# Kernel optimization log

Measured on AMD Instinct MI355X. Metric: run time of the kernel, lower is better.

## Reference

```python
import jax, jax.numpy as jnp
import numpy as np

C = 64
CQ = C // 8


def setup_inputs() -> dict:
    key = jax.random.key(0)
    ks = jax.random.split(key, 8)
    x = jax.random.normal(ks[0], (8, C, 64, 64), dtype=jnp.float32)
    s = 1.0 / np.sqrt(C)
    Wq = jax.random.normal(ks[1], (CQ, C), dtype=jnp.float32) * s
    bq = jax.random.normal(ks[2], (CQ,), dtype=jnp.float32) * s
    Wk = jax.random.normal(ks[3], (CQ, C), dtype=jnp.float32) * s
    bk = jax.random.normal(ks[4], (CQ,), dtype=jnp.float32) * s
    Wv = jax.random.normal(ks[5], (C, C), dtype=jnp.float32) * s
    bv = jax.random.normal(ks[6], (C,), dtype=jnp.float32) * s
    gamma = jnp.array([0.5], dtype=jnp.float32)  # nonzero so value path contributes
    return {"x": x, "Wq": Wq, "bq": bq, "Wk": Wk, "bk": bk, "Wv": Wv, "bv": bv, "gamma": gamma}


def reference(x, Wq, bq, Wk, bk, Wv, bv, gamma):
    B, Cc, H, W = x.shape
    xf = x.reshape(B, Cc, H * W)  # [B, C, N]
    # 1x1 conv == channel-mixing linear
    f = jnp.einsum('oc,bcn->bon', Wq, xf) + bq[None, :, None]  # [B, C/8, N]
    g = jnp.einsum('oc,bcn->bon', Wk, xf) + bk[None, :, None]  # [B, C/8, N]
    h = jnp.einsum('oc,bcn->bon', Wv, xf) + bv[None, :, None]  # [B, C, N]
    # scores[b,i,j] = f[b,:,i] . g[b,:,j]; softmax over dim=1 (query dim i)
    scores = jnp.einsum('bdi,bdj->bij', f, g)  # [B, N, N]
    beta = jax.nn.softmax(scores, axis=1)
    o = gamma[0] * jnp.einsum('bcn,bnm->bcm', h, beta) + xf
    return o.reshape(B, Cc, H, W)
```

## Files before the change

kernel.cpp:

```cpp
#include <hip/hip_runtime.h>
#include <hip/hip_fp16.h>


typedef _Float16 half8_t __attribute__((ext_vector_type(8)));
typedef _Float16 half4_t __attribute__((ext_vector_type(4)));
typedef _Float16 half2_t __attribute__((ext_vector_type(2)));
typedef __fp16  fp16x2  __attribute__((ext_vector_type(2)));
typedef float float4_t __attribute__((ext_vector_type(4)));

#define NTOK 4096
#define PRH 72
#define LOG2E 1.44269504088896340736f

#if __has_builtin(__builtin_amdgcn_exp2f)
__device__ __forceinline__ float fexp2(float x) { return __builtin_amdgcn_exp2f(x); }
#else
__device__ __forceinline__ float fexp2(float x) { return exp2f(x); }
#endif

__device__ __forceinline__ half2_t pkcvt(float a, float b) {
    fp16x2 v = __builtin_amdgcn_cvt_pkrtz(a, b);
    return __builtin_bit_cast(half2_t, v);
}

#define GLDS(G, L) __builtin_amdgcn_global_load_lds(                            \
    (const __attribute__((address_space(1))) unsigned int*)(G),                 \
    (__attribute__((address_space(3))) unsigned int*)(L), 16, 0, 0)

__global__ __launch_bounds__(320) void proj_kernel(
    const float* __restrict__ x,
    const float* __restrict__ Wq, const float* __restrict__ bq,
    const float* __restrict__ Wk, const float* __restrict__ bk,
    const float* __restrict__ Wv, const float* __restrict__ bv,
    __half* __restrict__ fTR, __half* __restrict__ gT16, __half* __restrict__ hM)
{
    __shared__ __align__(16) _Float16 xh[32 * PRH];
    const int t      = threadIdx.x;
    const int blk    = blockIdx.x;
    const int b      = blockIdx.y;
    const int n0     = blk * 32;
    const int kt64   = blk >> 1;
    const int t4base = (blk & 1) * 2;

    if (t < 256) {
#pragma unroll
        for (int i = 0; i < 2; i++) {
            const int idx = t + i * 256;
            const int c = idx >> 3, f4 = idx & 7;
            float4 v = *(const float4*)(x + (((size_t)(b * 64 + c)) << 12) + n0 + f4 * 4);
            const int cs = c ^ ((f4 & 3) << 4);
            xh[(f4 * 4 + 0) * PRH + cs] = (_Float16)v.x;
            xh[(f4 * 4 + 1) * PRH + cs] = (_Float16)v.y;
            xh[(f4 * 4 + 2) * PRH + cs] = (_Float16)v.z;
            xh[(f4 * 4 + 3) * PRH + cs] = (_Float16)v.w;
        }
    }

    const int w    = t >> 6;
    const int lane = t & 63;
    const int q    = lane >> 4;
    const int ml   = lane & 15;

    const float* wrow;
    if (w == 0) wrow = (ml < 8) ? (Wq + ml * 64) : (Wk + (ml - 8) * 64);
    else        wrow = Wv + ((w - 1) * 16 + ml) * 64;
    half4_t afr[4];
#pragma unroll
    for (int ks = 0; ks < 4; ks++) {
        float4 wv4 = *(const float4*)(wrow + ks * 16 + q * 4);
        afr[ks] = (half4_t){(_Float16)wv4.x, (_Float16)wv4.y,
                            (_Float16)wv4.z, (_Float16)wv4.w};
    }
    float4 bias4;
    if (w == 0) bias4 = (q < 2) ? *(const float4*)(bq + q * 4)
                                : *(const float4*)(bk + (q - 2) * 4);
    else        bias4 = *(const float4*)(bv + (w - 1) * 16 + q * 4);

    __syncthreads();

#pragma unroll
    for (int cg = 0; cg < 2; cg++) {
        const int tok  = cg * 16 + ml;
        const int swz  = (tok >> 2) & 3;
        float4_t acc = (float4_t){0.f, 0.f, 0.f, 0.f};
#pragma unroll
        for (int ks = 0; ks < 4; ks++) {
            half4_t bfr = *(const half4_t*)(&xh[tok * PRH + ((ks ^ swz) * 16 + q * 4)]);
            acc = __builtin_amdgcn_mfma_f32_16x16x16f16(afr[ks], bfr, acc, 0, 0, 0);
        }
        acc[0] += bias4.x; acc[1] += bias4.y; acc[2] += bias4.z; acc[3] += bias4.w;
        const int gtok = n0 + tok;
        const int t4   = t4base + cg;

        if (w == 0) {
            __half* rec = fTR + ((size_t)b << 16) + (size_t)(kt64 * 16 + ml) * 64;
            if (q < 2) {
                half4_t fv = {(_Float16)(acc[0] * LOG2E), (_Float16)(acc[1] * LOG2E),
                              (_Float16)(acc[2] * LOG2E), (_Float16)(acc[3] * LOG2E)};
                *(half4_t*)(rec + q * 16 + t4 * 4) = fv;
            } else {
                half4_t cv = (half4_t){};
                if (q == 2) cv[0] = (_Float16)1.0f;
                *(half4_t*)(rec + q * 16 + t4 * 4) = cv;
            }
            float gn2p = acc[0] * acc[0] + acc[1] * acc[1] +
                         acc[2] * acc[2] + acc[3] * acc[3];
            float gn2 = gn2p + __shfl_xor(gn2p, 16, 64);
            if (q >= 2) {
                half4_t gv = {(_Float16)acc[0], (_Float16)acc[1],
                              (_Float16)acc[2], (_Float16)acc[3]};
                __half* gp = gT16 + (size_t)((b << 12) + gtok) * 16;
                *(half4_t*)(gp + (q - 2) * 4) = gv;
                if (q == 2) {
                    const float M = (LOG2E * 4.6f) * __builtin_sqrtf(gn2) + 1.0f;
                    *(half4_t*)(gp + 8) = (half4_t){(_Float16)(-M), 0, 0, 0};
                } else {
                    *(half4_t*)(gp + 12) = (half4_t){};
                }
            }
        } else {
            const int ch  = (w - 1) * 16 + q * 4;
            const int pos = ((t4 >> 1) << 5) + ((ml >> 2) << 3) + ((t4 & 1) << 2) + (ml & 3);
            const size_t rowbase = ((size_t)(b * 64 + ch) << 12) + (size_t)kt64 * 64 + pos;
#pragma unroll
            for (int r = 0; r < 4; r++)
                hM[rowbase + ((size_t)r << 12)] = __float2half(acc[r]);
        }
    }
}

#define PAIR(SEA, SOA, SEB, SOB, GOFF)                                          \
    {                                                                           \
        const _Float16* hp = hb + (GOFF);                                       \
        half8_t ah0 = *(const half8_t*)(hp);                                    \
        half8_t ah1 = *(const half8_t*)(hp + 1024);                             \
        half8_t ah2 = *(const half8_t*)(hp + 2048);                             \
        half8_t ah3 = *(const half8_t*)(hp + 3072);                             \
        float eA0 = fexp2(SEA[0]), eA1 = fexp2(SEA[1]),                         \
              eA2 = fexp2(SEA[2]), eA3 = fexp2(SEA[3]);                         \
        float oA0 = fexp2(SOA[0]), oA1 = fexp2(SOA[1]),                         \
              oA2 = fexp2(SOA[2]), oA3 = fexp2(SOA[3]);                         \
        float eB0 = fexp2(SEB[0]), eB1 = fexp2(SEB[1]),                         \
              eB2 = fexp2(SEB[2]), eB3 = fexp2(SEB[3]);                         \
        float oB0 = fexp2(SOB[0]), oB1 = fexp2(SOB[1]),                         \
              oB2 = fexp2(SOB[2]), oB3 = fexp2(SOB[3]);                         \
        half2_t eaA = pkcvt(eA0, eA1), ebA = pkcvt(eA2, eA3);                   \
        half2_t oaA = pkcvt(oA0, oA1), obA = pkcvt(oA2, oA3);                   \
        half2_t eaB = pkcvt(eB0, eB1), ebB = pkcvt(eB2, eB3);                   \
        half2_t oaB = pkcvt(oB0, oB1), obB = pkcvt(oB2, oB3);                   \
        half8_t pA8 = {eaA[0], eaA[1], ebA[0], ebA[1],                          \
                       oaA[0], oaA[1], obA[0], obA[1]};                         \
        half8_t pB8 = {eaB[0], eaB[1], ebB[0], ebB[1],                          \
                       oaB[0], oaB[1], obB[0], obB[1]};                         \
        __builtin_amdgcn_s_setprio(1);                                          \
        accLA = __builtin_amdgcn_mfma_f32_16x16x32_f16(ones8, pA8, accLA, 0, 0, 0); \
        accLB = __builtin_amdgcn_mfma_f32_16x16x32_f16(ones8, pB8, accLB, 0, 0, 0); \
        accA[0] = __builtin_amdgcn_mfma_f32_16x16x32_f16(ah0, pA8, accA[0], 0, 0, 0); \
        accB[0] = __builtin_amdgcn_mfma_f32_16x16x32_f16(ah0, pB8, accB[0], 0, 0, 0); \
        accA[1] = __builtin_amdgcn_mfma_f32_16x16x32_f16(ah1, pA8, accA[1], 0, 0, 0); \
        accB[1] = __builtin_amdgcn_mfma_f32_16x16x32_f16(ah1, pB8, accB[1], 0, 0, 0); \
        accA[2] = __builtin_amdgcn_mfma_f32_16x16x32_f16(ah2, pA8, accA[2], 0, 0, 0); \
        accB[2] = __builtin_amdgcn_mfma_f32_16x16x32_f16(ah2, pB8, accB[2], 0, 0, 0); \
        accA[3] = __builtin_amdgcn_mfma_f32_16x16x32_f16(ah3, pA8, accA[3], 0, 0, 0); \
        accB[3] = __builtin_amdgcn_mfma_f32_16x16x32_f16(ah3, pB8, accB[3], 0, 0, 0); \
        __builtin_amdgcn_s_setprio(0);                                          \
    }

template<int NT>
__global__ __launch_bounds__(256) void attn_kernel(
    const __half* __restrict__ fTR, const __half* __restrict__ gT16,
    const __half* __restrict__ hM,
    __half* __restrict__ Pacc, float* __restrict__ Lsum)
{
    __shared__ __align__(16) _Float16 hl[2][4096];
    const int tid   = threadIdx.x;
    const int w     = tid >> 6;
    const int lane  = tid & 63;
    const int q     = lane >> 4;
    const int ml    = lane & 15;
    const int m7    = ml & 7;
    const int b     = blockIdx.y;
    const int split = blockIdx.z;
    const int colA  = blockIdx.x * 128 + w * 16 + ml;
    const int colB  = colA + 64;

    half4_t gfA = *(const half4_t*)(gT16 + ((size_t)((b << 12) + colA)) * 16 + q * 4);
    half4_t gfB = *(const half4_t*)(gT16 + ((size_t)((b << 12) + colB)) * 16 + q * 4);

    float4_t accA[4], accB[4];
#pragma unroll
    for (int cg = 0; cg < 4; cg++) {
        accA[cg] = (float4_t){0.f, 0.f, 0.f, 0.f};
        accB[cg] = (float4_t){0.f, 0.f, 0.f, 0.f};
    }
    float4_t accLA = (float4_t){0.f, 0.f, 0.f, 0.f};
    float4_t accLB = (float4_t){0.f, 0.f, 0.f, 0.f};
    const half8_t ones8 = {(_Float16)1.0f, (_Float16)1.0f, (_Float16)1.0f,
                           (_Float16)1.0f, (_Float16)1.0f, (_Float16)1.0f,
                           (_Float16)1.0f, (_Float16)1.0f};

    const int kt0 = split * NT;

    const int ch0  = tid >> 3;
    const int gsw  = (tid & 7) ^ (ch0 & 7);
    const __half* hs0 = hM + ((size_t)(b * 64 + ch0) << 12) + (size_t)kt0 * 64 + gsw * 8;
    const __half* hs1 = hs0 + ((size_t)32 << 12);
    const __half* fptr = fTR + ((size_t)b << 16) + (size_t)(kt0 * 16 + ml) * 64 + q * 16;

    const int gx0 = ((q ^ m7) << 3);
    const int gx1 = (((4 + q) ^ m7) << 3);

    GLDS(hs0, &hl[0][tid * 8]);
    GLDS(hs1, &hl[0][2048 + tid * 8]);
    half8_t f01 = *(const half8_t*)fptr;
    half8_t f23 = *(const half8_t*)(fptr + 8);
    __syncthreads();

#pragma unroll 1
    for (int kt = 0; kt < NT; kt++) {
        if (kt + 1 < NT) {
            _Float16* nb = &hl[(kt + 1) & 1][0];
            GLDS(hs0 + (kt + 1) * 64, nb + tid * 8);
            GLDS(hs1 + (kt + 1) * 64, nb + 2048 + tid * 8);
        }

        const _Float16* hb = &hl[kt & 1][ml << 6];
        half4_t afn0 = __builtin_shufflevector(f01, f01, 0, 1, 2, 3);
        half4_t afn1 = __builtin_shufflevector(f01, f01, 4, 5, 6, 7);
        half4_t afn2 = __builtin_shufflevector(f23, f23, 0, 1, 2, 3);
        half4_t afn3 = __builtin_shufflevector(f23, f23, 4, 5, 6, 7);

        __builtin_amdgcn_s_setprio(1);
        float4_t stA0 = __builtin_amdgcn_mfma_f32_16x16x16f16(
            afn0, gfA, (float4_t){0.f, 0.f, 0.f, 0.f}, 0, 0, 0);
        float4_t stA1 = __builtin_amdgcn_mfma_f32_16x16x16f16(
            afn1, gfA, (float4_t){0.f, 0.f, 0.f, 0.f}, 0, 0, 0);
        float4_t stA2 = __builtin_amdgcn_mfma_f32_16x16x16f16(
            afn2, gfA, (float4_t){0.f, 0.f, 0.f, 0.f}, 0, 0, 0);
        float4_t stA3 = __builtin_amdgcn_mfma_f32_16x16x16f16(
            afn3, gfA, (float4_t){0.f, 0.f, 0.f, 0.f}, 0, 0, 0);
        float4_t stB0 = __builtin_amdgcn_mfma_f32_16x16x16f16(
            afn0, gfB, (float4_t){0.f, 0.f, 0.f, 0.f}, 0, 0, 0);
        float4_t stB1 = __builtin_amdgcn_mfma_f32_16x16x16f16(
            afn1, gfB, (float4_t){0.f, 0.f, 0.f, 0.f}, 0, 0, 0);
        float4_t stB2 = __builtin_amdgcn_mfma_f32_16x16x16f16(
            afn2, gfB, (float4_t){0.f, 0.f, 0.f, 0.f}, 0, 0, 0);
        float4_t stB3 = __builtin_amdgcn_mfma_f32_16x16x16f16(
            afn3, gfB, (float4_t){0.f, 0.f, 0.f, 0.f}, 0, 0, 0);
        __builtin_amdgcn_s_setprio(0);

        if (kt + 1 < NT) {
            f01 = *(const half8_t*)(fptr + 1024);
            f23 = *(const half8_t*)(fptr + 1032);
            fptr += 1024;
        }

        PAIR(stA0, stA1, stB0, stB1, gx0)
        PAIR(stA2, stA3, stB2, stB3, gx1)

        __syncthreads();
    }

    __half* pa = Pacc + (((size_t)(split * 8 + b) * 64) << 12);
#pragma unroll
    for (int cg = 0; cg < 4; cg++)
#pragma unroll
        for (int r = 0; r < 4; r++) {
            int ch = cg * 16 + q * 4 + r;
            pa[((size_t)ch << 12) + colA] = __float2half(accA[cg][r]);
            pa[((size_t)ch << 12) + colB] = __float2half(accB[cg][r]);
        }
    if (q == 0) {
        Lsum[((size_t)(split * 8 + b) << 12) + colA] = accLA[0];
        Lsum[((size_t)(split * 8 + b) << 12) + colB] = accLB[0];
    }
}

template<int S>
__global__ __launch_bounds__(256) void merge_kernel(
    const __half* __restrict__ Pacc, const float* __restrict__ Lsum,
    const float* __restrict__ x, const float* __restrict__ gammap,
    float* __restrict__ out)
{
    __shared__ float invL[64];
    const int tid  = threadIdx.x;
    const int c4   = tid & 15;
    const int chh  = tid >> 4;
    const int b    = blockIdx.y;
    const int col0 = blockIdx.x * 64;
    const int ch   = blockIdx.z * 16 + chh;

    if (tid < 64) {
        float L = 0.f;
#pragma unroll
        for (int s = 0; s < S; s++)
            L += Lsum[((size_t)(s * 8 + b) << 12) + col0 + tid];
        invL[tid] = gammap[0] / L;
    }
    __syncthreads();

    const int cc = c4 * 4;
    const size_t base = (((size_t)b * 64 + ch) << 12) + col0 + cc;
    float4 xv = *(const float4*)(x + base);
    float o0 = 0.f, o1 = 0.f, o2 = 0.f, o3 = 0.f;
#pragma unroll
    for (int s = 0; s < S; s++) {
        half4_t pv = *(const half4_t*)(Pacc +
            (((size_t)(s * 8 + b) * 64 + ch) << 12) + col0 + cc);
        o0 += (float)pv[0];
        o1 += (float)pv[1];
        o2 += (float)pv[2];
        o3 += (float)pv[3];
    }
    float4 ov;
    ov.x = o0 * invL[cc]     + xv.x;
    ov.y = o1 * invL[cc + 1] + xv.y;
    ov.z = o2 * invL[cc + 2] + xv.z;
    ov.w = o3 * invL[cc + 3] + xv.w;
    *(float4*)(out + base) = ov;
}

extern "C" void kernel_launch(void* const* d_in, const int* in_sizes, int n_in,
                              void* d_out, int out_size, void* d_ws, size_t ws_size,
                              hipStream_t stream) {
    const float* x     = (const float*)d_in[0];
    const float* Wq    = (const float*)d_in[1];
    const float* bq    = (const float*)d_in[2];
    const float* Wk    = (const float*)d_in[3];
    const float* bk    = (const float*)d_in[4];
    const float* Wv    = (const float*)d_in[5];
    const float* bv    = (const float*)d_in[6];
    const float* gamma = (const float*)d_in[7];
    float* out = (float*)d_out;

    const size_t fr_bytes  = (size_t)8 * 65536 * 2;
    const size_t g_bytes   = (size_t)8 * NTOK * 16 * 2;
    const size_t hM_bytes  = (size_t)8 * 64 * NTOK * 2;
    const size_t pa_split  = (size_t)8 * 64 * NTOK * 2;
    const size_t l_split   = (size_t)8 * NTOK * sizeof(float);
    const size_t base_need = fr_bytes + g_bytes + hM_bytes;

    int S = 1;
    if (ws_size >= base_need + 8 * (pa_split + l_split)) S = 8;
    else if (ws_size >= base_need + 4 * (pa_split + l_split)) S = 4;
    else if (ws_size >= base_need + 2 * (pa_split + l_split)) S = 2;

    char* p = (char*)d_ws;
    __half* fTR  = (__half*)p;  p += fr_bytes;
    __half* gT16 = (__half*)p;  p += g_bytes;
    __half* hM   = (__half*)p;  p += hM_bytes;
    __half* Pacc = (__half*)p;  p += (size_t)S * pa_split;
    float*  Lsum = (float*)p;

    proj_kernel<<<dim3(128, 8), 320, 0, stream>>>(x, Wq, bq, Wk, bk, Wv, bv,
                                                  fTR, gT16, hM);
    if (S == 8) {
        attn_kernel<8><<<dim3(32, 8, 8), 256, 0, stream>>>(fTR, gT16, hM, Pacc, Lsum);
        merge_kernel<8><<<dim3(64, 8, 4), 256, 0, stream>>>(Pacc, Lsum, x, gamma, out);
    } else if (S == 4) {
        attn_kernel<16><<<dim3(32, 8, 4), 256, 0, stream>>>(fTR, gT16, hM, Pacc, Lsum);
        merge_kernel<4><<<dim3(64, 8, 4), 256, 0, stream>>>(Pacc, Lsum, x, gamma, out);
    } else if (S == 2) {
        attn_kernel<32><<<dim3(32, 8, 2), 256, 0, stream>>>(fTR, gT16, hM, Pacc, Lsum);
        merge_kernel<2><<<dim3(64, 8, 4), 256, 0, stream>>>(Pacc, Lsum, x, gamma, out);
    } else {
        attn_kernel<64><<<dim3(32, 8, 1), 256, 0, stream>>>(fTR, gT16, hM, Pacc, Lsum);
        merge_kernel<1><<<dim3(64, 8, 4), 256, 0, stream>>>(Pacc, Lsum, x, gamma, out);
    }
}
```

Baseline: 119.7 us.

## Triple-buffer attention LDS loads with vmcnt waits and drop 8-way split

Moves the attention kernel's value-tile staging from double to triple buffering in shared memory. Tiles are prefetched two iterations ahead, and the full __syncthreads is replaced by an explicit s_waitcnt vmcnt(2) plus s_barrier, so later loads can stay in flight while the current tile is consumed. It also removes the 8-way key split, so the maximum is 4 splits of 16 tiles each, which means fewer blocks and a smaller partial-sum merge. Shared memory per block grows and occupancy may drop; the vmcnt count relies on exactly how many loads are outstanding.

```diff
diff --git a/kernel.cpp b/kernel.cpp
--- a/kernel.cpp
+++ b/kernel.cpp
@@ -26,6 +26,13 @@
 #define GLDS(G, L) __builtin_amdgcn_global_load_lds(                            \
     (const __attribute__((address_space(1))) unsigned int*)(G),                 \
     (__attribute__((address_space(3))) unsigned int*)(L), 16, 0, 0)
+
+#define WAITVM2_BAR() do {                                                      \
+    __builtin_amdgcn_sched_barrier(0);                                          \
+    asm volatile("s_waitcnt vmcnt(2)" ::: "memory");                            \
+    __builtin_amdgcn_sched_barrier(0);                                          \
+    __builtin_amdgcn_s_barrier();                                               \
+} while (0)
 
 __global__ __launch_bounds__(320) void proj_kernel(
     const float* __restrict__ x,
@@ -172,7 +179,7 @@
     const __half* __restrict__ hM,
     __half* __restrict__ Pacc, float* __restrict__ Lsum)
 {
-    __shared__ __align__(16) _Float16 hl[2][4096];
+    __shared__ __align__(16) _Float16 hl[3][4096];
     const int tid   = threadIdx.x;
     const int w     = tid >> 6;
     const int lane  = tid & 63;
@@ -210,21 +217,21 @@
     const int gx0 = ((q ^ m7) << 3);
     const int gx1 = (((4 + q) ^ m7) << 3);
 
-    GLDS(hs0, &hl[0][tid * 8]);
-    GLDS(hs1, &hl[0][2048 + tid * 8]);
+    _Float16* bcur = &hl[0][0];
+    _Float16* bnxt = &hl[1][0];
+    _Float16* bnx2 = &hl[2][0];
+
+    GLDS(hs0, bcur + tid * 8);
+    GLDS(hs1, bcur + 2048 + tid * 8);
     half8_t f01 = *(const half8_t*)fptr;
     half8_t f23 = *(const half8_t*)(fptr + 8);
-    __syncthreads();
+    GLDS(hs0 + 64, bnxt + tid * 8);
+    GLDS(hs1 + 64, bnxt + 2048 + tid * 8);
+    WAITVM2_BAR();
 
 #pragma unroll 1
     for (int kt = 0; kt < NT; kt++) {
-        if (kt + 1 < NT) {
-            _Float16* nb = &hl[(kt + 1) & 1][0];
-            GLDS(hs0 + (kt + 1) * 64, nb + tid * 8);
-            GLDS(hs1 + (kt + 1) * 64, nb + 2048 + tid * 8);
-        }
-
-        const _Float16* hb = &hl[kt & 1][ml << 6];
+        const _Float16* hb = bcur + (ml << 6);
         half4_t afn0 = __builtin_shufflevector(f01, f01, 0, 1, 2, 3);
         half4_t afn1 = __builtin_shufflevector(f01, f01, 4, 5, 6, 7);
         half4_t afn2 = __builtin_shufflevector(f23, f23, 0, 1, 2, 3);
@@ -254,11 +261,18 @@
             f23 = *(const half8_t*)(fptr + 1032);
             fptr += 1024;
         }
+        if (kt + 2 < NT) {
+            GLDS(hs0 + (kt + 2) * 64, bnx2 + tid * 8);
+            GLDS(hs1 + (kt + 2) * 64, bnx2 + 2048 + tid * 8);
+        }
 
         PAIR(stA0, stA1, stB0, stB1, gx0)
         PAIR(stA2, stA3, stB2, stB3, gx1)
 
-        __syncthreads();
+        if (kt + 1 < NT) {
+            WAITVM2_BAR();
+            _Float16* tmp = bcur; bcur = bnxt; bnxt = bnx2; bnx2 = tmp;
+        }
     }
 
     __half* pa = Pacc + (((size_t)(split * 8 + b) * 64) << 12);
@@ -341,8 +355,7 @@
     const size_t base_need = fr_bytes + g_bytes + hM_bytes;
 
     int S = 1;
-    if (ws_size >= base_need + 8 * (pa_split + l_split)) S = 8;
-    else if (ws_size >= base_need + 4 * (pa_split + l_split)) S = 4;
+    if (ws_size >= base_need + 4 * (pa_split + l_split)) S = 4;
     else if (ws_size >= base_need + 2 * (pa_split + l_split)) S = 2;
 
     char* p = (char*)d_ws;
@@ -354,10 +367,7 @@
 
     proj_kernel<<<dim3(128, 8), 320, 0, stream>>>(x, Wq, bq, Wk, bk, Wv, bv,
                                                   fTR, gT16, hM);
-    if (S == 8) {
-        attn_kernel<8><<<dim3(32, 8, 8), 256, 0, stream>>>(fTR, gT16, hM, Pacc, Lsum);
-        merge_kernel<8><<<dim3(64, 8, 4), 256, 0, stream>>>(Pacc, Lsum, x, gamma, out);
-    } else if (S == 4) {
+    if (S == 4) {
         attn_kernel<16><<<dim3(32, 8, 4), 256, 0, stream>>>(fTR, gT16, hM, Pacc, Lsum);
         merge_kernel<4><<<dim3(64, 8, 4), 256, 0, stream>>>(Pacc, Lsum, x, gamma, out);
     } else if (S == 2) {
```

Result: no change. 118.5 us (-1.0%).

## Replace ones-MFMA row sums with scalar adds and interleave score/PV phases

Applied to the files above, without the earlier changes.

Drops the two ones-vector MFMAs per pair that computed softmax denominators. Column sums are now accumulated with VALU adds in fp32 and reduced across quads with shuffles at the end. The loop interleaves the score MFMAs with the exp/PV work, and the block-wide __syncthreads is replaced by a partial vmcnt(2) wait plus s_barrier so the in-flight global-to-LDS prefetch is not fully drained. Occupancy is hinted at 8 blocks via launch bounds, which risks register spills. Summing in fp32 instead of from fp16-rounded values slightly changes the numerics.

```diff
diff --git a/kernel.cpp b/kernel.cpp
--- a/kernel.cpp
+++ b/kernel.cpp
@@ -23,9 +23,23 @@
     return __builtin_bit_cast(half2_t, v);
 }
 
+__device__ __forceinline__ float4_t mfma16(half4_t a, half4_t b, float4_t c) {
+    return __builtin_amdgcn_mfma_f32_16x16x16f16(a, b, c, 0, 0, 0);
+}
+__device__ __forceinline__ float4_t mfma32(half8_t a, half8_t b, float4_t c) {
+    return __builtin_amdgcn_mfma_f32_16x16x32_f16(a, b, c, 0, 0, 0);
+}
+
 #define GLDS(G, L) __builtin_amdgcn_global_load_lds(                            \
     (const __attribute__((address_space(1))) unsigned int*)(G),                 \
     (__attribute__((address_space(3))) unsigned int*)(L), 16, 0, 0)
+
+#define WAITVM2_BAR() do {                                                      \
+    __builtin_amdgcn_sched_barrier(0);                                          \
+    asm volatile("s_waitcnt vmcnt(2)" ::: "memory");                            \
+    __builtin_amdgcn_sched_barrier(0);                                          \
+    __builtin_amdgcn_s_barrier();                                               \
+} while (0)
 
 __global__ __launch_bounds__(320) void proj_kernel(
     const float* __restrict__ x,
@@ -134,8 +148,6 @@
         const _Float16* hp = hb + (GOFF);                                       \
         half8_t ah0 = *(const half8_t*)(hp);                                    \
         half8_t ah1 = *(const half8_t*)(hp + 1024);                             \
-        half8_t ah2 = *(const half8_t*)(hp + 2048);                             \
-        half8_t ah3 = *(const half8_t*)(hp + 3072);                             \
         float eA0 = fexp2(SEA[0]), eA1 = fexp2(SEA[1]),                         \
               eA2 = fexp2(SEA[2]), eA3 = fexp2(SEA[3]);                         \
         float oA0 = fexp2(SOA[0]), oA1 = fexp2(SOA[1]),                         \
@@ -144,6 +156,12 @@
               eB2 = fexp2(SEB[2]), eB3 = fexp2(SEB[3]);                         \
         float oB0 = fexp2(SOB[0]), oB1 = fexp2(SOB[1]),                         \
               oB2 = fexp2(SOB[2]), oB3 = fexp2(SOB[3]);                         \
+        lpA0 += (eA0 + eA1) + (eA2 + eA3);                                      \
+        lpA1 += (oA0 + oA1) + (oA2 + oA3);                                      \
+        lpB0 += (eB0 + eB1) + (eB2 + eB3);                                      \
+        lpB1 += (oB0 + oB1) + (oB2 + oB3);                                      \
+        half8_t ah2 = *(const half8_t*)(hp + 2048);                             \
+        half8_t ah3 = *(const half8_t*)(hp + 3072);                             \
         half2_t eaA = pkcvt(eA0, eA1), ebA = pkcvt(eA2, eA3);                   \
         half2_t oaA = pkcvt(oA0, oA1), obA = pkcvt(oA2, oA3);                   \
         half2_t eaB = pkcvt(eB0, eB1), ebB = pkcvt(eB2, eB3);                   \
@@ -153,21 +171,15 @@
         half8_t pB8 = {eaB[0], eaB[1], ebB[0], ebB[1],                          \
                        oaB[0], oaB[1], obB[0], obB[1]};                         \
         __builtin_amdgcn_s_setprio(1);                                          \
-        accLA = __builtin_amdgcn_mfma_f32_16x16x32_f16(ones8, pA8, accLA, 0, 0, 0); \
-        accLB = __builtin_amdgcn_mfma_f32_16x16x32_f16(ones8, pB8, accLB, 0, 0, 0); \
-        accA[0] = __builtin_amdgcn_mfma_f32_16x16x32_f16(ah0, pA8, accA[0], 0, 0, 0); \
-        accB[0] = __builtin_amdgcn_mfma_f32_16x16x32_f16(ah0, pB8, accB[0], 0, 0, 0); \
-        accA[1] = __builtin_amdgcn_mfma_f32_16x16x32_f16(ah1, pA8, accA[1], 0, 0, 0); \
-        accB[1] = __builtin_amdgcn_mfma_f32_16x16x32_f16(ah1, pB8, accB[1], 0, 0, 0); \
-        accA[2] = __builtin_amdgcn_mfma_f32_16x16x32_f16(ah2, pA8, accA[2], 0, 0, 0); \
-        accB[2] = __builtin_amdgcn_mfma_f32_16x16x32_f16(ah2, pB8, accB[2], 0, 0, 0); \
-        accA[3] = __builtin_amdgcn_mfma_f32_16x16x32_f16(ah3, pA8, accA[3], 0, 0, 0); \
-        accB[3] = __builtin_amdgcn_mfma_f32_16x16x32_f16(ah3, pB8, accB[3], 0, 0, 0); \
+        accA[0] = mfma32(ah0, pA8, accA[0]); accB[0] = mfma32(ah0, pB8, accB[0]); \
+        accA[1] = mfma32(ah1, pA8, accA[1]); accB[1] = mfma32(ah1, pB8, accB[1]); \
+        accA[2] = mfma32(ah2, pA8, accA[2]); accB[2] = mfma32(ah2, pB8, accB[2]); \
+        accA[3] = mfma32(ah3, pA8, accA[3]); accB[3] = mfma32(ah3, pB8, accB[3]); \
         __builtin_amdgcn_s_setprio(0);                                          \
     }
 
 template<int NT>
-__global__ __launch_bounds__(256) void attn_kernel(
+__global__ __launch_bounds__(256, 8) void attn_kernel(
     const __half* __restrict__ fTR, const __half* __restrict__ gT16,
     const __half* __restrict__ hM,
     __half* __restrict__ Pacc, float* __restrict__ Lsum)
@@ -193,11 +205,8 @@
         accA[cg] = (float4_t){0.f, 0.f, 0.f, 0.f};
         accB[cg] = (float4_t){0.f, 0.f, 0.f, 0.f};
     }
-    float4_t accLA = (float4_t){0.f, 0.f, 0.f, 0.f};
-    float4_t accLB = (float4_t){0.f, 0.f, 0.f, 0.f};
-    const half8_t ones8 = {(_Float16)1.0f, (_Float16)1.0f, (_Float16)1.0f,
-                           (_Float16)1.0f, (_Float16)1.0f, (_Float16)1.0f,
-                           (_Float16)1.0f, (_Float16)1.0f};
+    float lpA0 = 0.f, lpA1 = 0.f, lpB0 = 0.f, lpB1 = 0.f;
+    const float4_t z4 = (float4_t){0.f, 0.f, 0.f, 0.f};
 
     const int kt0 = split * NT;
 
@@ -207,8 +216,8 @@
     const __half* hs1 = hs0 + ((size_t)32 << 12);
     const __half* fptr = fTR + ((size_t)b << 16) + (size_t)(kt0 * 16 + ml) * 64 + q * 16;
 
-    const int gx0 = ((q ^ m7) << 3);
-    const int gx1 = (((4 + q) ^ m7) << 3);
+    const int gxa = ((q ^ m7) << 3);
+    const int gxb = (((4 + q) ^ m7) << 3);
 
     GLDS(hs0, &hl[0][tid * 8]);
     GLDS(hs1, &hl[0][2048 + tid * 8]);
@@ -231,22 +240,19 @@
         half4_t afn3 = __builtin_shufflevector(f23, f23, 4, 5, 6, 7);
 
         __builtin_amdgcn_s_setprio(1);
-        float4_t stA0 = __builtin_amdgcn_mfma_f32_16x16x16f16(
-            afn0, gfA, (float4_t){0.f, 0.f, 0.f, 0.f}, 0, 0, 0);
-        float4_t stA1 = __builtin_amdgcn_mfma_f32_16x16x16f16(
-            afn1, gfA, (float4_t){0.f, 0.f, 0.f, 0.f}, 0, 0, 0);
-        float4_t stA2 = __builtin_amdgcn_mfma_f32_16x16x16f16(
-            afn2, gfA, (float4_t){0.f, 0.f, 0.f, 0.f}, 0, 0, 0);
-        float4_t stA3 = __builtin_amdgcn_mfma_f32_16x16x16f16(
-            afn3, gfA, (float4_t){0.f, 0.f, 0.f, 0.f}, 0, 0, 0);
-        float4_t stB0 = __builtin_amdgcn_mfma_f32_16x16x16f16(
-            afn0, gfB, (float4_t){0.f, 0.f, 0.f, 0.f}, 0, 0, 0);
-        float4_t stB1 = __builtin_amdgcn_mfma_f32_16x16x16f16(
-            afn1, gfB, (float4_t){0.f, 0.f, 0.f, 0.f}, 0, 0, 0);
-        float4_t stB2 = __builtin_amdgcn_mfma_f32_16x16x16f16(
-            afn2, gfB, (float4_t){0.f, 0.f, 0.f, 0.f}, 0, 0, 0);
-        float4_t stB3 = __builtin_amdgcn_mfma_f32_16x16x16f16(
-            afn3, gfB, (float4_t){0.f, 0.f, 0.f, 0.f}, 0, 0, 0);
+        float4_t stA0 = mfma16(afn0, gfA, z4);
+        float4_t stB0 = mfma16(afn0, gfB, z4);
+        float4_t stA1 = mfma16(afn1, gfA, z4);
+        float4_t stB1 = mfma16(afn1, gfB, z4);
+        __builtin_amdgcn_s_setprio(0);
+
+        PAIR(stA0, stA1, stB0, stB1, gxa)
+
+        __builtin_amdgcn_s_setprio(1);
+        float4_t stA2 = mfma16(afn2, gfA, z4);
+        float4_t stB2 = mfma16(afn2, gfB, z4);
+        float4_t stA3 = mfma16(afn3, gfA, z4);
+        float4_t stB3 = mfma16(afn3, gfB, z4);
         __builtin_amdgcn_s_setprio(0);
 
         if (kt + 1 < NT) {
@@ -255,11 +261,19 @@
             fptr += 1024;
         }
 
-        PAIR(stA0, stA1, stB0, stB1, gx0)
-        PAIR(stA2, stA3, stB2, stB3, gx1)
-
-        __syncthreads();
-    }
+        PAIR(stA2, stA3, stB2, stB3, gxb)
+
+        if (kt + 1 < NT) {
+            WAITVM2_BAR();
+        }
+    }
+
+    float lA = lpA0 + lpA1;
+    lA += __shfl_xor(lA, 16, 64);
+    lA += __shfl_xor(lA, 32, 64);
+    float lB = lpB0 + lpB1;
+    lB += __shfl_xor(lB, 16, 64);
+    lB += __shfl_xor(lB, 32, 64);
 
     __half* pa = Pacc + (((size_t)(split * 8 + b) * 64) << 12);
 #pragma unroll
@@ -271,8 +285,8 @@
             pa[((size_t)ch << 12) + colB] = __float2half(accB[cg][r]);
         }
     if (q == 0) {
-        Lsum[((size_t)(split * 8 + b) << 12) + colA] = accLA[0];
-        Lsum[((size_t)(split * 8 + b) << 12) + colB] = accLB[0];
+        Lsum[((size_t)(split * 8 + b) << 12) + colA] = lA;
+        Lsum[((size_t)(split * 8 + b) << 12) + colB] = lB;
     }
 }
 
```

Result: slower. 431.4 us (+260.5%).
